# Kernel tuning notes

Hardware: AMD Instinct MI355X
Metric: run time of the kernel (lower is better)

## Reference

```python
import jax, jax.numpy as jnp
import numpy as np

# dims
B, S = 1, 32768          # batch, grid seqlen (32^3 latent grid)
NQ, NE = 32768, 262144   # mesh query nodes, grid->query edges
IN, EMB, HID, BOT, PREDH, OUT, NDIM = 192, 192, 192, 192, 192, 4, 3
MAX_WAVELENGTH = 10000.0


def sincos_embed(coords, dim, ndim):
    # ContinuousSincosEmbed: dim % ndim == 0 and (dim//ndim) even here -> no padding
    eff = dim // ndim                                     # 64 dims per coordinate
    omega = 1.0 / MAX_WAVELENGTH ** (jnp.arange(0, eff, 2, dtype=jnp.float32) / eff)  # [eff//2]
    out = coords[..., None] * omega                       # [N, ndim, eff//2]
    emb = jnp.concatenate([jnp.sin(out), jnp.cos(out)], axis=-1)  # [N, ndim, eff]
    return emb.reshape(coords.shape[0], ndim * eff)       # [N, dim]


def _linear_params(key, fan_in, fan_out):
    k1, k2 = jax.random.split(key)
    lim = 1.0 / np.sqrt(fan_in)
    w = jax.random.uniform(k1, (fan_in, fan_out), jnp.float32, -lim, lim)
    b = jax.random.uniform(k2, (fan_out,), jnp.float32, -lim, lim)
    return w, b


def setup_inputs() -> dict:
    key = jax.random.key(0)
    ks = jax.random.split(key, 10)
    x = jax.random.normal(ks[0], (B, S, IN), jnp.float32)
    query_pos = jax.random.uniform(ks[1], (NQ, NDIM), jnp.float32) * 100.0
    # edges sorted by query index (required by the CSR segment reduce in the original)
    qidx = jnp.sort(jax.random.randint(ks[2], (NE,), 0, NQ))
    gidx = jax.random.randint(ks[3], (NE,), 0, B * S)
    grid_to_query_edges = jnp.stack([qidx, gidx], axis=1).astype(jnp.int64)
    proj_w, proj_b = _linear_params(ks[4], IN, EMB)
    msg0_w, msg0_b = _linear_params(ks[5], 2 * EMB, 2 * HID)
    msg1_w, msg1_b = _linear_params(ks[6], 2 * HID, 2 * HID)
    msg2_w, msg2_b = _linear_params(ks[7], 2 * HID, BOT)
    pred0_w, pred0_b = _linear_params(ks[8], BOT, PREDH)
    pred1_w, pred1_b = _linear_params(ks[9], PREDH, OUT)
    return dict(x=x, query_pos=query_pos, grid_to_query_edges=grid_to_query_edges,
                proj_w=proj_w, proj_b=proj_b,
                msg0_w=msg0_w, msg0_b=msg0_b, msg1_w=msg1_w, msg1_b=msg1_b,
                msg2_w=msg2_w, msg2_b=msg2_b,
                pred0_w=pred0_w, pred0_b=pred0_b, pred1_w=pred1_w, pred1_b=pred1_b)


def reference(x, query_pos, grid_to_query_edges,
              proj_w, proj_b, msg0_w, msg0_b, msg1_w, msg1_b, msg2_w, msg2_b,
              pred0_w, pred0_b, pred1_w, pred1_b):
    gelu = lambda t: jax.nn.gelu(t, approximate=False)  # torch nn.GELU default (erf)
    # flatten grid tokens and project
    xf = x.reshape(-1, x.shape[-1]) @ proj_w + proj_b          # [B*S, EMB]
    qe = sincos_embed(query_pos, EMB, NDIM)                    # [NQ, EMB]
    qidx = grid_to_query_edges[:, 0]
    gidx = grid_to_query_edges[:, 1]
    # gather + concat per edge
    h = jnp.concatenate([xf[gidx], qe[qidx]], axis=1)          # [NE, 2*EMB]
    # message MLP
    h = gelu(h @ msg0_w + msg0_b)
    h = gelu(h @ msg1_w + msg1_b)
    h = h @ msg2_w + msg2_b                                    # [NE, BOT]
    # segment mean to query nodes (empty segments -> 0, matching segment_csr mean)
    nq = query_pos.shape[0]
    seg_sum = jax.ops.segment_sum(h, qidx, num_segments=nq)    # [NQ, BOT]
    cnt = jax.ops.segment_sum(jnp.ones((qidx.shape[0], 1), h.dtype), qidx, num_segments=nq)
    m = seg_sum / jnp.maximum(cnt, 1.0)
    # prediction head
    out = gelu(m @ pred0_w + pred0_b) @ pred1_w + pred1_b      # [NQ, OUT]
    return out
```

## Files before the change

### kernel.cpp

```cpp
#include <hip/hip_runtime.h>
#include <math.h>

#define N_Q    32768
#define N_E    262144

typedef _Float16 half8 __attribute__((ext_vector_type(8)));
typedef _Float16 half4v __attribute__((ext_vector_type(4)));
typedef float f32x4 __attribute__((ext_vector_type(4)));

__device__ __forceinline__ float gelu_f(float x) {
    float ax = fabsf(x);
    float t = __builtin_amdgcn_rcpf(fmaf(0.33269070724668f, ax, 1.0f));
    float poly = t * fmaf(t, fmaf(t, 0.7478556f, -0.0958798f), 0.3480242f);
    float e = exp2f(-0.72134752044448f * ax * ax);
    float u = fmaf(-poly, e, 1.0f);
    return 0.5f * fmaf(ax, u, x);
}

__global__ __launch_bounds__(256) void embed_kernel(const float* __restrict__ qpos,
                                                    _Float16* __restrict__ qe) {
    int gid = blockIdx.x * 256 + threadIdx.x;
    int q = gid / 96, r = gid - q * 96;
    int d = r >> 5, i = r & 31;
    float omega = exp2f(-(float)i * 0.41524101186092029f);
    float arg = qpos[q * 3 + d] * omega;
    float rev = arg * 0.15915494309189535f;
    rev = rev - floorf(rev);
    float s = __builtin_amdgcn_sinf(rev);
    float c = __builtin_amdgcn_cosf(rev);
    int base = q * 192 + d * 64 + i;
    qe[base] = (_Float16)s;
    qe[base + 32] = (_Float16)c;
}

__device__ __forceinline__ void pack_one(const float* __restrict__ W,
                                         _Float16* __restrict__ Wp,
                                         int K, int N, int blk0, int tid) {
    int u = blk0 * 256 + tid;
    if (u * 8 >= K * N) return;
    int l = u & 63, blk = u >> 6;
    int nks = K >> 5;
    int ntile = blk / nks, ks = blk - ntile * nks;
    int n = ntile * 16 + (l & 15);
    int k0 = ks * 32 + (l >> 4) * 8;
    half8 v;
    #pragma unroll
    for (int j = 0; j < 8; ++j) v[j] = (_Float16)W[(size_t)(k0 + j) * N + n];
    *(half8*)(Wp + (size_t)u * 8) = v;
}

__global__ __launch_bounds__(256) void pack_all_kernel(
    const float* __restrict__ pw,  _Float16* __restrict__ WpP,
    const float* __restrict__ m0,  _Float16* __restrict__ Wp0,
    const float* __restrict__ m1,  _Float16* __restrict__ Wp1,
    const float* __restrict__ m2,  _Float16* __restrict__ Wp2,
    const float* __restrict__ hw,  _Float16* __restrict__ WpH) {
    int b = blockIdx.x, t = threadIdx.x;
    if      (b < 18)  pack_one(pw, WpP, 192, 192, b,        t);
    else if (b < 90)  pack_one(m0, Wp0, 384, 384, b - 18,   t);
    else if (b < 162) pack_one(m1, Wp1, 384, 384, b - 90,   t);
    else if (b < 198) pack_one(m2, Wp2, 384, 192, b - 162,  t);
    else              pack_one(hw, WpH, 192, 192, b - 198,  t);
}

#define PK 200

__global__ __launch_bounds__(256, 2) void proj_mfma_kernel(
    const float* __restrict__ x, const _Float16* __restrict__ Wp,
    const float* __restrict__ bias, _Float16* __restrict__ xf)
{
    __shared__ _Float16 hA[64 * PK];
    const int t = threadIdx.x;
    const int r0 = blockIdx.x * 64;
    const int lane = t & 63;
    const int w = t >> 6;
    const int ln = lane & 15, lq = lane >> 4;

    #pragma unroll
    for (int i = 0; i < 12; ++i) {
        int idx = t + 256 * i;
        int r = idx / 48, c4 = idx - r * 48;
        float4 v = ((const float4*)(x + (size_t)(r0 + r) * 192))[c4];
        half4v hv; hv[0] = (_Float16)v.x; hv[1] = (_Float16)v.y;
        hv[2] = (_Float16)v.z; hv[3] = (_Float16)v.w;
        *(half4v*)(hA + r * PK + c4 * 4) = hv;
    }
    __syncthreads();

    f32x4 acc[4][3];
    #pragma unroll
    for (int nt = 0; nt < 3; ++nt) {
        float bv = bias[w * 48 + nt * 16 + ln];
        #pragma unroll
        for (int mt = 0; mt < 4; ++mt) acc[mt][nt] = (f32x4){bv, bv, bv, bv};
    }
    #pragma unroll 2
    for (int ks = 0; ks < 6; ++ks) {
        half8 a[4], bf[3];
        #pragma unroll
        for (int mt = 0; mt < 4; ++mt)
            a[mt] = *(const half8*)(hA + (mt * 16 + ln) * PK + ks * 32 + lq * 8);
        #pragma unroll
        for (int nt = 0; nt < 3; ++nt)
            bf[nt] = *(const half8*)(Wp + (size_t)(((w * 3 + nt) * 6 + ks) * 512 + lane * 8));
        #pragma unroll
        for (int nt = 0; nt < 3; ++nt)
            #pragma unroll
            for (int mt = 0; mt < 4; ++mt)
                acc[mt][nt] = __builtin_amdgcn_mfma_f32_16x16x32_f16(a[mt], bf[nt], acc[mt][nt], 0, 0, 0);
    }
    #pragma unroll
    for (int mt = 0; mt < 4; ++mt)
        #pragma unroll
        for (int nt = 0; nt < 3; ++nt)
            #pragma unroll
            for (int r = 0; r < 4; ++r) {
                int m = mt * 16 + lq * 4 + r;
                int n = w * 48 + nt * 16 + ln;
                xf[(size_t)(r0 + m) * 192 + n] = (_Float16)acc[mt][nt][r];
            }
}

#define PADK 392

__global__ __launch_bounds__(512, 6) void edge_mlp_kernel(
    const _Float16* __restrict__ xf, const _Float16* __restrict__ qe,
    const int* __restrict__ edges,
    const _Float16* __restrict__ Wp0, const float* __restrict__ b0,
    const _Float16* __restrict__ Wp1, const float* __restrict__ b1,
    const _Float16* __restrict__ Wp2, const float* __restrict__ b2,
    float* __restrict__ seg, float* __restrict__ cnt)
{
    __shared__ _Float16 hA[64 * PADK];
    __shared__ int qi[64], gi[64];
    float* h2 = (float*)hA;

    const int t = threadIdx.x;
    const int e0 = blockIdx.x * 64;
    const int lane = t & 63;
    const int w = t >> 6;
    const int ln = lane & 15;
    const int lq = lane >> 4;

    if (t < 64) {
        qi[t] = edges[2 * (e0 + t)];
        gi[t] = edges[2 * (e0 + t) + 1];
    }
    __syncthreads();

    #pragma unroll
    for (int i = 0; i < 6; ++i) {
        int idx = t + 512 * i;
        int m = idx / 48, c = idx - m * 48;
        const half8* src = (c < 24) ? ((const half8*)(xf + (size_t)gi[m] * 192) + c)
                                    : ((const half8*)(qe + (size_t)qi[m] * 192) + (c - 24));
        *(half8*)(hA + m * PADK + c * 8) = *src;
    }
    __syncthreads();

    #pragma unroll 1
    for (int L = 0; L < 2; ++L) {
        const _Float16* __restrict__ Wp = L ? Wp1 : Wp0;
        const float* __restrict__ bias = L ? b1 : b0;

        f32x4 acc[4][3];
        #pragma unroll
        for (int nt = 0; nt < 3; ++nt) {
            float bv = bias[w * 48 + nt * 16 + ln];
            #pragma unroll
            for (int mt = 0; mt < 4; ++mt)
                acc[mt][nt] = (f32x4){bv, bv, bv, bv};
        }
        #pragma unroll 2
        for (int ks = 0; ks < 12; ++ks) {
            half8 a[4], bf[3];
            #pragma unroll
            for (int mt = 0; mt < 4; ++mt)
                a[mt] = *(const half8*)(hA + (mt * 16 + ln) * PADK + ks * 32 + lq * 8);
            #pragma unroll
            for (int nt = 0; nt < 3; ++nt)
                bf[nt] = *(const half8*)(Wp + (size_t)(((w * 3 + nt) * 12 + ks) * 512 + lane * 8));
            #pragma unroll
            for (int nt = 0; nt < 3; ++nt)
                #pragma unroll
                for (int mt = 0; mt < 4; ++mt)
                    acc[mt][nt] = __builtin_amdgcn_mfma_f32_16x16x32_f16(a[mt], bf[nt], acc[mt][nt], 0, 0, 0);
        }
        __syncthreads();
        #pragma unroll
        for (int mt = 0; mt < 4; ++mt)
            #pragma unroll
            for (int nt = 0; nt < 3; ++nt)
                #pragma unroll
                for (int r = 0; r < 4; ++r) {
                    int m = mt * 16 + lq * 4 + r;
                    int n = w * 48 + nt * 16 + ln;
                    hA[m * PADK + n] = (_Float16)gelu_f(acc[mt][nt][r]);
                }
        __syncthreads();
    }

    {
        const int n0 = (w & 3) * 48;
        const int mh = (w >> 2) * 2;
        f32x4 acc[2][3];
        #pragma unroll
        for (int nt = 0; nt < 3; ++nt) {
            float bv = b2[n0 + nt * 16 + ln];
            #pragma unroll
            for (int mt = 0; mt < 2; ++mt)
                acc[mt][nt] = (f32x4){bv, bv, bv, bv};
        }
        #pragma unroll 2
        for (int ks = 0; ks < 12; ++ks) {
            half8 a[2], bf[3];
            #pragma unroll
            for (int mt = 0; mt < 2; ++mt)
                a[mt] = *(const half8*)(hA + ((mh + mt) * 16 + ln) * PADK + ks * 32 + lq * 8);
            #pragma unroll
            for (int nt = 0; nt < 3; ++nt)
                bf[nt] = *(const half8*)(Wp2 + (size_t)((((w & 3) * 3 + nt) * 12 + ks) * 512 + lane * 8));
            #pragma unroll
            for (int nt = 0; nt < 3; ++nt)
                #pragma unroll
                for (int mt = 0; mt < 2; ++mt)
                    acc[mt][nt] = __builtin_amdgcn_mfma_f32_16x16x32_f16(a[mt], bf[nt], acc[mt][nt], 0, 0, 0);
        }
        __syncthreads();
        #pragma unroll
        for (int mt = 0; mt < 2; ++mt)
            #pragma unroll
            for (int nt = 0; nt < 3; ++nt)
                #pragma unroll
                for (int r = 0; r < 4; ++r) {
                    int m = (mh + mt) * 16 + lq * 4 + r;
                    int n = n0 + nt * 16 + ln;
                    h2[m * 192 + n] = acc[mt][nt][r];
                }
        __syncthreads();
    }

    if (t < 384) {
        int half = t >= 192;
        int col = t - half * 192;
        int mlo = half * 32, mhi = mlo + 32;
        float a = 0.0f;
        for (int m = mlo; m < mhi; ++m) {
            a += h2[m * 192 + col];
            if (m == mhi - 1 || qi[m + 1] != qi[m]) {
                atomicAdd(&seg[(size_t)qi[m] * 192 + col], a);
                a = 0.0f;
            }
        }
    } else if (t < 386) {
        int half = t - 384;
        int mlo = half * 32, mhi = mlo + 32;
        float run = 1.0f;
        for (int m = mlo + 1; m < mhi; ++m) {
            if (qi[m] != qi[m - 1]) { atomicAdd(&cnt[qi[m - 1]], run); run = 1.0f; }
            else run += 1.0f;
        }
        atomicAdd(&cnt[qi[mhi - 1]], run);
    }
}

#define PSK 196

__global__ __launch_bounds__(256, 2) void head_kernel(
    const float* __restrict__ seg, const float* __restrict__ cnt,
    const _Float16* __restrict__ Wp0, const float* __restrict__ b0,
    const float* __restrict__ w1, const float* __restrict__ b1,
    float* __restrict__ out)
{
    __shared__ _Float16 hA[64 * PK];
    __shared__ float ps[64 * PSK];
    __shared__ float w1s[192 * 4];
    __shared__ float invc[64];
    const int t = threadIdx.x;
    const int r0 = blockIdx.x * 64;
    const int lane = t & 63;
    const int w = t >> 6;
    const int ln = lane & 15, lq = lane >> 4;

    if (t < 64) invc[t] = 1.0f / fmaxf(cnt[r0 + t], 1.0f);
    if (t < 192) ((float4*)w1s)[t] = ((const float4*)w1)[t];
    __syncthreads();

    #pragma unroll
    for (int i = 0; i < 12; ++i) {
        int idx = t + 256 * i;
        int r = idx / 48, c4 = idx - r * 48;
        float inv = invc[r];
        float4 v = ((const float4*)(seg + (size_t)(r0 + r) * 192))[c4];
        half4v hv; hv[0] = (_Float16)(v.x * inv); hv[1] = (_Float16)(v.y * inv);
        hv[2] = (_Float16)(v.z * inv); hv[3] = (_Float16)(v.w * inv);
        *(half4v*)(hA + r * PK + c4 * 4) = hv;
    }
    __syncthreads();

    f32x4 acc[4][3];
    #pragma unroll
    for (int nt = 0; nt < 3; ++nt) {
        float bv = b0[w * 48 + nt * 16 + ln];
        #pragma unroll
        for (int mt = 0; mt < 4; ++mt) acc[mt][nt] = (f32x4){bv, bv, bv, bv};
    }
    #pragma unroll 2
    for (int ks = 0; ks < 6; ++ks) {
        half8 a[4], bf[3];
        #pragma unroll
        for (int mt = 0; mt < 4; ++mt)
            a[mt] = *(const half8*)(hA + (mt * 16 + ln) * PK + ks * 32 + lq * 8);
        #pragma unroll
        for (int nt = 0; nt < 3; ++nt)
            bf[nt] = *(const half8*)(Wp0 + (size_t)(((w * 3 + nt) * 6 + ks) * 512 + lane * 8));
        #pragma unroll
        for (int nt = 0; nt < 3; ++nt)
            #pragma unroll
            for (int mt = 0; mt < 4; ++mt)
                acc[mt][nt] = __builtin_amdgcn_mfma_f32_16x16x32_f16(a[mt], bf[nt], acc[mt][nt], 0, 0, 0);
    }
    #pragma unroll
    for (int mt = 0; mt < 4; ++mt)
        #pragma unroll
        for (int nt = 0; nt < 3; ++nt)
            #pragma unroll
            for (int r = 0; r < 4; ++r) {
                int m = mt * 16 + lq * 4 + r;
                int n = w * 48 + nt * 16 + ln;
                ps[m * PSK + n] = gelu_f(acc[mt][nt][r]);
            }
    __syncthreads();

    {
        int r = t >> 2, oo = t & 3;
        float a = b1[oo];
        for (int k = 0; k < 192; ++k)
            a = fmaf(ps[r * PSK + k], w1s[k * 4 + oo], a);
        out[(size_t)(r0 + r) * 4 + oo] = a;
    }
}

extern "C" void kernel_launch(void* const* d_in, const int* in_sizes, int n_in,
                              void* d_out, int out_size, void* d_ws, size_t ws_size,
                              hipStream_t stream) {
    (void)in_sizes; (void)n_in; (void)out_size; (void)ws_size;
    const float* x       = (const float*)d_in[0];
    const float* qpos    = (const float*)d_in[1];
    const int*   edges   = (const int*)d_in[2];
    const float* proj_w  = (const float*)d_in[3];
    const float* proj_b  = (const float*)d_in[4];
    const float* msg0_w  = (const float*)d_in[5];
    const float* msg0_b  = (const float*)d_in[6];
    const float* msg1_w  = (const float*)d_in[7];
    const float* msg1_b  = (const float*)d_in[8];
    const float* msg2_w  = (const float*)d_in[9];
    const float* msg2_b  = (const float*)d_in[10];
    const float* pred0_w = (const float*)d_in[11];
    const float* pred0_b = (const float*)d_in[12];
    const float* pred1_w = (const float*)d_in[13];
    const float* pred1_b = (const float*)d_in[14];
    float* out = (float*)d_out;

    char* ws = (char*)d_ws;
    _Float16* xf  = (_Float16*)(ws);
    _Float16* qe  = (_Float16*)(ws + 12582912);
    float*    seg = (float*)(ws + 25165824);
    float*    cnt = (float*)(ws + 50331648);
    _Float16* Wp0 = (_Float16*)(ws + 50462720);
    _Float16* Wp1 = (_Float16*)(ws + 50757632);
    _Float16* Wp2 = (_Float16*)(ws + 51052544);
    _Float16* WpP = (_Float16*)(ws + 51200000);
    _Float16* WpH = (_Float16*)(ws + 51273728);

    hipMemsetAsync(seg, 0, 25165824 + 131072, stream);
    embed_kernel<<<12288, 256, 0, stream>>>(qpos, qe);
    pack_all_kernel<<<216, 256, 0, stream>>>(proj_w, WpP, msg0_w, Wp0,
                                             msg1_w, Wp1, msg2_w, Wp2,
                                             pred0_w, WpH);
    proj_mfma_kernel<<<512, 256, 0, stream>>>(x, WpP, proj_b, xf);
    edge_mlp_kernel<<<4096, 512, 0, stream>>>(xf, qe, edges,
                                              Wp0, msg0_b, Wp1, msg1_b, Wp2, msg2_b,
                                              seg, cnt);
    head_kernel<<<512, 256, 0, stream>>>(seg, cnt, WpH, pred0_b,
                                         pred1_w, pred1_b, out);
}
```

Baseline: 367.9 us.

## Swap MFMA operands to get transposed accumulators for vectorized stores and gather

Swaps the A/B operands of every MFMA so each lane's accumulator holds four consecutive output columns for one row. Bias loads and epilogue stores (xf, hA, h2, ps) become 4-wide vector writes instead of scalar strided writes. The edge kernel gather is restructured so each thread reads its edge's int2 directly and copies contiguous row chunks, removing the gi shared array and one barrier. h2 gets a padded stride to reduce LDS bank conflicts in the vector stores, at the cost of relying on the padded stride fitting within the hA buffer.

After: 384.0 us. 1.04x slower.

```diff
diff --git a/kernel.cpp b/kernel.cpp
--- a/kernel.cpp
+++ b/kernel.cpp
@@ -90,9 +90,9 @@
     f32x4 acc[4][3];
     #pragma unroll
     for (int nt = 0; nt < 3; ++nt) {
-        float bv = bias[w * 48 + nt * 16 + ln];
-        #pragma unroll
-        for (int mt = 0; mt < 4; ++mt) acc[mt][nt] = (f32x4){bv, bv, bv, bv};
+        f32x4 bv = *(const f32x4*)(bias + w * 48 + nt * 16 + lq * 4);
+        #pragma unroll
+        for (int mt = 0; mt < 4; ++mt) acc[mt][nt] = bv;
     }
     #pragma unroll 2
     for (int ks = 0; ks < 6; ++ks) {
@@ -107,21 +107,21 @@
         for (int nt = 0; nt < 3; ++nt)
             #pragma unroll
             for (int mt = 0; mt < 4; ++mt)
-                acc[mt][nt] = __builtin_amdgcn_mfma_f32_16x16x32_f16(a[mt], bf[nt], acc[mt][nt], 0, 0, 0);
+                acc[mt][nt] = __builtin_amdgcn_mfma_f32_16x16x32_f16(bf[nt], a[mt], acc[mt][nt], 0, 0, 0);
     }
     #pragma unroll
     for (int mt = 0; mt < 4; ++mt)
         #pragma unroll
-        for (int nt = 0; nt < 3; ++nt)
-            #pragma unroll
-            for (int r = 0; r < 4; ++r) {
-                int m = mt * 16 + lq * 4 + r;
-                int n = w * 48 + nt * 16 + ln;
-                xf[(size_t)(r0 + m) * 192 + n] = (_Float16)acc[mt][nt][r];
-            }
+        for (int nt = 0; nt < 3; ++nt) {
+            half4v hv;
+            #pragma unroll
+            for (int r = 0; r < 4; ++r) hv[r] = (_Float16)acc[mt][nt][r];
+            *(half4v*)(xf + (size_t)(r0 + mt * 16 + ln) * 192 + w * 48 + nt * 16 + lq * 4) = hv;
+        }
 }
 
 #define PADK 392
+#define H2S  196
 
 __global__ __launch_bounds__(512, 6) void edge_mlp_kernel(
     const _Float16* __restrict__ xf, const _Float16* __restrict__ qe,
@@ -132,7 +132,7 @@
     float* __restrict__ seg, float* __restrict__ cnt)
 {
     __shared__ _Float16 hA[64 * PADK];
-    __shared__ int qi[64], gi[64];
+    __shared__ int qi[64];
     float* h2 = (float*)hA;
 
     const int t = threadIdx.x;
@@ -142,19 +142,19 @@
     const int ln = lane & 15;
     const int lq = lane >> 4;
 
-    if (t < 64) {
-        qi[t] = edges[2 * (e0 + t)];
-        gi[t] = edges[2 * (e0 + t) + 1];
-    }
-    __syncthreads();
-
-    #pragma unroll
-    for (int i = 0; i < 6; ++i) {
-        int idx = t + 512 * i;
-        int m = idx / 48, c = idx - m * 48;
-        const half8* src = (c < 24) ? ((const half8*)(xf + (size_t)gi[m] * 192) + c)
-                                    : ((const half8*)(qe + (size_t)qi[m] * 192) + (c - 24));
-        *(half8*)(hA + m * PADK + c * 8) = *src;
+    if (t < 64) qi[t] = edges[2 * (e0 + t)];
+
+    {
+        const int m = t >> 3;
+        const int cl = t & 7;
+        int2 eg = ((const int2*)edges)[e0 + m];
+        const half8* xsrc = (const half8*)(xf + (size_t)eg.y * 192) + cl;
+        const half8* qsrc = (const half8*)(qe + (size_t)eg.x * 192) + cl;
+        half8* dst = (half8*)(hA + m * PADK + cl * 8);
+        #pragma unroll
+        for (int i = 0; i < 3; ++i) dst[i * 8] = xsrc[i * 8];
+        #pragma unroll
+        for (int i = 0; i < 3; ++i) dst[24 + i * 8] = qsrc[i * 8];
     }
     __syncthreads();
 
@@ -166,10 +166,9 @@
         f32x4 acc[4][3];
         #pragma unroll
         for (int nt = 0; nt < 3; ++nt) {
-            float bv = bias[w * 48 + nt * 16 + ln];
-            #pragma unroll
-            for (int mt = 0; mt < 4; ++mt)
-                acc[mt][nt] = (f32x4){bv, bv, bv, bv};
+            f32x4 bv = *(const f32x4*)(bias + w * 48 + nt * 16 + lq * 4);
+            #pragma unroll
+            for (int mt = 0; mt < 4; ++mt) acc[mt][nt] = bv;
         }
         #pragma unroll 2
         for (int ks = 0; ks < 12; ++ks) {
@@ -184,19 +183,18 @@
             for (int nt = 0; nt < 3; ++nt)
                 #pragma unroll
                 for (int mt = 0; mt < 4; ++mt)
-                    acc[mt][nt] = __builtin_amdgcn_mfma_f32_16x16x32_f16(a[mt], bf[nt], acc[mt][nt], 0, 0, 0);
+                    acc[mt][nt] = __builtin_amdgcn_mfma_f32_16x16x32_f16(bf[nt], a[mt], acc[mt][nt], 0, 0, 0);
         }
         __syncthreads();
         #pragma unroll
         for (int mt = 0; mt < 4; ++mt)
             #pragma unroll
-            for (int nt = 0; nt < 3; ++nt)
+            for (int nt = 0; nt < 3; ++nt) {
+                half4v hv;
                 #pragma unroll
-                for (int r = 0; r < 4; ++r) {
-                    int m = mt * 16 + lq * 4 + r;
-                    int n = w * 48 + nt * 16 + ln;
-                    hA[m * PADK + n] = (_Float16)gelu_f(acc[mt][nt][r]);
-                }
+                for (int r = 0; r < 4; ++r) hv[r] = (_Float16)gelu_f(acc[mt][nt][r]);
+                *(half4v*)(hA + (mt * 16 + ln) * PADK + w * 48 + nt * 16 + lq * 4) = hv;
+            }
         __syncthreads();
     }
 
@@ -206,10 +204,9 @@
         f32x4 acc[2][3];
         #pragma unroll
         for (int nt = 0; nt < 3; ++nt) {
-            float bv = b2[n0 + nt * 16 + ln];
-            #pragma unroll
-            for (int mt = 0; mt < 2; ++mt)
-                acc[mt][nt] = (f32x4){bv, bv, bv, bv};
+            f32x4 bv = *(const f32x4*)(b2 + n0 + nt * 16 + lq * 4);
+            #pragma unroll
+            for (int mt = 0; mt < 2; ++mt) acc[mt][nt] = bv;
         }
         #pragma unroll 2
         for (int ks = 0; ks < 12; ++ks) {
@@ -224,37 +221,32 @@
             for (int nt = 0; nt < 3; ++nt)
                 #pragma unroll
                 for (int mt = 0; mt < 2; ++mt)
-                    acc[mt][nt] = __builtin_amdgcn_mfma_f32_16x16x32_f16(a[mt], bf[nt], acc[mt][nt], 0, 0, 0);
+                    acc[mt][nt] = __builtin_amdgcn_mfma_f32_16x16x32_f16(bf[nt], a[mt], acc[mt][nt], 0, 0, 0);
         }
         __syncthreads();
         #pragma unroll
         for (int mt = 0; mt < 2; ++mt)
             #pragma unroll
             for (int nt = 0; nt < 3; ++nt)
-                #pragma unroll
-                for (int r = 0; r < 4; ++r) {
-                    int m = (mh + mt) * 16 + lq * 4 + r;
-                    int n = n0 + nt * 16 + ln;
-                    h2[m * 192 + n] = acc[mt][nt][r];
-                }
+                *(f32x4*)(h2 + ((mh + mt) * 16 + ln) * H2S + n0 + nt * 16 + lq * 4) = acc[mt][nt];
         __syncthreads();
     }
 
     if (t < 384) {
-        int half = t >= 192;
-        int col = t - half * 192;
-        int mlo = half * 32, mhi = mlo + 32;
+        int half_ = t >= 192;
+        int col = t - half_ * 192;
+        int mlo = half_ * 32, mhi = mlo + 32;
         float a = 0.0f;
         for (int m = mlo; m < mhi; ++m) {
-            a += h2[m * 192 + col];
+            a += h2[m * H2S + col];
             if (m == mhi - 1 || qi[m + 1] != qi[m]) {
                 atomicAdd(&seg[(size_t)qi[m] * 192 + col], a);
                 a = 0.0f;
             }
         }
     } else if (t < 386) {
-        int half = t - 384;
-        int mlo = half * 32, mhi = mlo + 32;
+        int half_ = t - 384;
+        int mlo = half_ * 32, mhi = mlo + 32;
         float run = 1.0f;
         for (int m = mlo + 1; m < mhi; ++m) {
             if (qi[m] != qi[m - 1]) { atomicAdd(&cnt[qi[m - 1]], run); run = 1.0f; }
@@ -301,9 +293,9 @@
     f32x4 acc[4][3];
     #pragma unroll
     for (int nt = 0; nt < 3; ++nt) {
-        float bv = b0[w * 48 + nt * 16 + ln];
-        #pragma unroll
-        for (int mt = 0; mt < 4; ++mt) acc[mt][nt] = (f32x4){bv, bv, bv, bv};
+        f32x4 bv = *(const f32x4*)(b0 + w * 48 + nt * 16 + lq * 4);
+        #pragma unroll
+        for (int mt = 0; mt < 4; ++mt) acc[mt][nt] = bv;
     }
     #pragma unroll 2
     for (int ks = 0; ks < 6; ++ks) {
@@ -318,18 +310,17 @@
         for (int nt = 0; nt < 3; ++nt)
             #pragma unroll
             for (int mt = 0; mt < 4; ++mt)
-                acc[mt][nt] = __builtin_amdgcn_mfma_f32_16x16x32_f16(a[mt], bf[nt], acc[mt][nt], 0, 0, 0);
+                acc[mt][nt] = __builtin_amdgcn_mfma_f32_16x16x32_f16(bf[nt], a[mt], acc[mt][nt], 0, 0, 0);
     }
     #pragma unroll
     for (int mt = 0; mt < 4; ++mt)
         #pragma unroll
-        for (int nt = 0; nt < 3; ++nt)
-            #pragma unroll
-            for (int r = 0; r < 4; ++r) {
-                int m = mt * 16 + lq * 4 + r;
-                int n = w * 48 + nt * 16 + ln;
-                ps[m * PSK + n] = gelu_f(acc[mt][nt][r]);
-            }
+        for (int nt = 0; nt < 3; ++nt) {
+            f32x4 g;
+            #pragma unroll
+            for (int r = 0; r < 4; ++r) g[r] = gelu_f(acc[mt][nt][r]);
+            *(f32x4*)(ps + (mt * 16 + ln) * PSK + w * 48 + nt * 16 + lq * 4) = g;
+        }
     __syncthreads();
 
     {
```
